# Kernel tuning notes

Hardware: AMD Instinct MI355X
Metric: run time of the kernel (lower is better)

The kernel has to match this reference:

```python
import jax, jax.numpy as jnp
import numpy as np
import math

NUM_LEVEL = 16
LEVEL_DIM = 2
BASE_RES = 16
LOG2_T = 19
LEVEL_SCALE = 1.38191288
N_POINTS = 262144

_PRIMES = np.array([1, 2654435761, 805459861], dtype=np.uint32)  # tiny-cuda-nn hash primes
_CORNERS = np.array([[(c >> d) & 1 for d in range(3)] for c in range(8)], dtype=np.uint32)  # [8,3]


def _grid_meta():
    # mirrors GridEncoder.get_grid_info: per-level table offsets (aligned to 8)
    max_len = 2 ** LOG2_T
    offs = []
    off = 0
    for i in range(NUM_LEVEL):
        res = int(np.ceil(BASE_RES * LEVEL_SCALE ** i))
        p = min(max_len, res ** 3)
        p = int(np.ceil(p / 8) * 8)
        offs.append(off)
        off += p
    offs.append(off)
    return offs


def setup_inputs() -> dict:
    key = jax.random.key(0)
    k1, k2 = jax.random.split(key)
    offs = _grid_meta()
    # raw coords in [-1, 1); forward maps (x+1)/2 -> [0, 1)
    input_means = jax.random.uniform(k1, (N_POINTS, 3), dtype=jnp.float32) * 2.0 - 1.0
    # embeddings.data.uniform_(-0.01, 0.01)
    embeddings = jax.random.uniform(k2, (offs[-1], LEVEL_DIM), dtype=jnp.float32) * 0.02 - 0.01
    return {"input_means": input_means, "embeddings": embeddings}


def _encode(input_means, embeddings):
    x = (input_means + 1.0) / 2.0  # [N,3] in [0,1]
    offs = _grid_meta()
    lg_scale = math.log2(LEVEL_SCALE)
    corners = jnp.asarray(_CORNERS)  # [8,3]
    primes = jnp.asarray(_PRIMES)    # [3]
    outs = []
    for l in range(NUM_LEVEL):
        hsize = offs[l + 1] - offs[l]                    # table rows this level
        scale = 2.0 ** (l * lg_scale) * BASE_RES - 1.0   # align_corners=True
        res = int(math.ceil(scale)) + 1                  # grid resolution
        table = embeddings[offs[l]:offs[l + 1]]          # [hsize, C]
        pos = x * scale                                  # align_corners -> no +0.5
        pg = jnp.floor(pos)
        frac = pos - pg                                  # [N,3]
        pgu = pg.astype(jnp.uint32)
        cpos = pgu[:, None, :] + corners[None]           # [N,8,3] corner coords
        if res ** 3 > hsize:
            # hashed level: xor of coord*prime (uint32 wraparound)
            h = cpos * primes
            idx = h[..., 0] ^ h[..., 1] ^ h[..., 2]
        else:
            # dense (tiled) level
            r = jnp.uint32(res)
            idx = cpos[..., 0] + cpos[..., 1] * r + cpos[..., 2] * r * r
        idx = (idx % jnp.uint32(hsize)).astype(jnp.int32)
        feats = table[idx]                               # [N,8,C] gather
        w = jnp.where(corners[None] == 1, frac[:, None, :], 1.0 - frac[:, None, :]).prod(-1)  # [N,8]
        outs.append(jnp.einsum('nk,nkc->nc', w, feats))  # trilinear interp
    # matches ot_encod.permute(1,0,2).reshape(N, L*C): level-major feature concat
    return jnp.concatenate(outs, axis=-1)                # [N, L*C]


def reference(input_means, embeddings):
    return _encode(input_means, embeddings)
```

## Files before the change

kernel.cpp:

```cpp
#include <hip/hip_runtime.h>
#include <cmath>

#define NPTS 262144
#define NLVL 16
#define NDENSE 5
#define NHASH 11
#define HASH_MASK 0x7FFFFu

struct MetaD { float scale[NDENSE]; unsigned off[NDENSE]; unsigned res[NDENSE]; };
struct MetaH { float scale[NHASH]; unsigned off[NHASH]; };

__global__ __launch_bounds__(256) void enc_dense(
    const float* __restrict__ means, const float* __restrict__ emb,
    float2* __restrict__ dst, int lvl_major, MetaD meta)
{
    const int p = blockIdx.x * 256 + threadIdx.x;
    const int l = blockIdx.y;

    const float x = (means[3 * p + 0] + 1.0f) * 0.5f;
    const float y = (means[3 * p + 1] + 1.0f) * 0.5f;
    const float z = (means[3 * p + 2] + 1.0f) * 0.5f;

    const float s      = meta.scale[l];
    const unsigned off = meta.off[l];
    const unsigned r   = meta.res[l];

    const float px = x * s, py = y * s, pz = z * s;
    const float gx = floorf(px), gy = floorf(py), gz = floorf(pz);
    const float fx = px - gx, fy = py - gy, fz = pz - gz;
    const unsigned ix = (unsigned)gx, iy = (unsigned)gy, iz = (unsigned)gz;

    const unsigned base = ix + iy * r + iz * r * r + off;
    const unsigned dy = r, dz = r * r;

    const float2* __restrict__ emb2 = (const float2*)emb;
    float2 f[8];
    f[0] = emb2[base];           f[1] = emb2[base + 1];
    f[2] = emb2[base + dy];      f[3] = emb2[base + dy + 1];
    f[4] = emb2[base + dz];      f[5] = emb2[base + dz + 1];
    f[6] = emb2[base + dz + dy]; f[7] = emb2[base + dz + dy + 1];

    const float wx0 = 1.0f - fx, wy0 = 1.0f - fy, wz0 = 1.0f - fz;
    const float w00 = wz0 * wy0, w01 = wz0 * fy, w10 = fz * wy0, w11 = fz * fy;
    const float a0 = w00 * (wx0 * f[0].x + fx * f[1].x) + w01 * (wx0 * f[2].x + fx * f[3].x)
                   + w10 * (wx0 * f[4].x + fx * f[5].x) + w11 * (wx0 * f[6].x + fx * f[7].x);
    const float a1 = w00 * (wx0 * f[0].y + fx * f[1].y) + w01 * (wx0 * f[2].y + fx * f[3].y)
                   + w10 * (wx0 * f[4].y + fx * f[5].y) + w11 * (wx0 * f[6].y + fx * f[7].y);

    const size_t di = lvl_major ? ((size_t)l * NPTS + p) : ((size_t)p * NLVL + l);
    dst[di] = make_float2(a0, a1);
}

__device__ __forceinline__ float2 hash_level(
    const float* __restrict__ emb, unsigned off, float s,
    float x, float y, float z)
{
    const float px = x * s, py = y * s, pz = z * s;
    const float gx = floorf(px), gy = floorf(py), gz = floorf(pz);
    const float fx = px - gx, fy = py - gy, fz = pz - gz;
    const unsigned ix = (unsigned)gx, iy = (unsigned)gy, iz = (unsigned)gz;

    const unsigned hy0 = iy * 2654435761u, hy1 = hy0 + 2654435761u;
    const unsigned hz0 = iz * 805459861u,  hz1 = hz0 + 805459861u;
    const unsigned hyz[4] = {hy0 ^ hz0, hy1 ^ hz0, hy0 ^ hz1, hy1 ^ hz1};

    const float wy0 = 1.0f - fy, wz0 = 1.0f - fz;
    const float wc[4] = {wy0 * wz0, fy * wz0, wy0 * fz, fy * fz};
    const float wx0 = 1.0f - fx;

    const float2* __restrict__ emb2 = (const float2*)emb;
    const float4* __restrict__ emb4 = (const float4*)emb;

    float a0 = 0.0f, a1 = 0.0f;
    if ((ix & 1u) == 0u) {
#pragma unroll
        for (int c = 0; c < 4; ++c) {
            const unsigned i0 = (ix ^ hyz[c]) & HASH_MASK;
            const float4 f = emb4[(off + (i0 & ~1u)) >> 1];
            const bool sw = (i0 & 1u);
            const float c0x = sw ? f.z : f.x, c0y = sw ? f.w : f.y;
            const float c1x = sw ? f.x : f.z, c1y = sw ? f.y : f.w;
            a0 += wc[c] * (wx0 * c0x + fx * c1x);
            a1 += wc[c] * (wx0 * c0y + fx * c1y);
        }
    } else {
#pragma unroll
        for (int c = 0; c < 4; ++c) {
            const unsigned i0 = (ix        ^ hyz[c]) & HASH_MASK;
            const unsigned i1 = ((ix + 1u) ^ hyz[c]) & HASH_MASK;
            const float2 f0 = emb2[off + i0];
            const float2 f1 = emb2[off + i1];
            a0 += wc[c] * (wx0 * f0.x + fx * f1.x);
            a1 += wc[c] * (wx0 * f0.y + fx * f1.y);
        }
    }
    return make_float2(a0, a1);
}

__global__ __launch_bounds__(256) void enc_hash(
    const float* __restrict__ means, const float* __restrict__ emb,
    float2* __restrict__ dst, int lvl_major, MetaH meta)
{
    const unsigned b = blockIdx.x;
    const unsigned xcd = b & 7u, slot = b >> 3;
    unsigned il, chunk;
    if (slot < 512u) { il = xcd; chunk = slot; }
    else {
        if (xcd >= 6u) return;
        il = 8u + (xcd >> 1);
        chunk = ((slot - 512u) << 1) | (xcd & 1u);
    }
    const float s      = meta.scale[il];
    const unsigned off = meta.off[il];
    const unsigned lvl = il + NDENSE;

    const unsigned p0 = chunk * 512u + threadIdx.x;

#pragma unroll
    for (int pp = 0; pp < 2; ++pp) {
        const unsigned p = p0 + pp * 256u;
        const float x = (means[3 * p + 0] + 1.0f) * 0.5f;
        const float y = (means[3 * p + 1] + 1.0f) * 0.5f;
        const float z = (means[3 * p + 2] + 1.0f) * 0.5f;
        const float2 a = hash_level(emb, off, s, x, y, z);
        const size_t di = lvl_major ? ((size_t)lvl * NPTS + p) : ((size_t)p * NLVL + lvl);
        dst[di] = a;
    }
}

__global__ __launch_bounds__(256) void transpose_out(
    const float2* __restrict__ ws, float* __restrict__ out)
{
    const int p = blockIdx.x * 256 + threadIdx.x;
    float4 o[8];
    float2* o2 = (float2*)o;
#pragma unroll
    for (int l = 0; l < NLVL; ++l)
        o2[l] = ws[(size_t)l * NPTS + p];
    float4* out4 = (float4*)(out + (size_t)p * (2 * NLVL));
#pragma unroll
    for (int k = 0; k < 8; ++k)
        out4[k] = o[k];
}

extern "C" void kernel_launch(void* const* d_in, const int* in_sizes, int n_in,
                              void* d_out, int out_size, void* d_ws, size_t ws_size,
                              hipStream_t stream)
{
    const float* means = (const float*)d_in[0];
    const float* emb   = (const float*)d_in[1];
    float* out         = (float*)d_out;

    MetaD md;
    MetaH mh;
    const double lg = log2(1.38191288);
    unsigned off = 0;
    for (int l = 0; l < NLVL; ++l) {
        const double scale_d = pow(2.0, (double)l * lg) * 16.0 - 1.0;
        const unsigned res_enc = (unsigned)ceil(scale_d) + 1u;

        const double gres_d = ceil(16.0 * pow(1.38191288, (double)l));
        unsigned long long r3 = (unsigned long long)gres_d;
        r3 = r3 * r3 * r3;
        unsigned long long pl = r3 < (1ull << 19) ? r3 : (1ull << 19);
        pl = (pl + 7ull) / 8ull * 8ull;

        if (l < NDENSE) {
            md.scale[l] = (float)scale_d;
            md.off[l]   = off;
            md.res[l]   = res_enc;
        } else {
            mh.scale[l - NDENSE] = (float)scale_d;
            mh.off[l - NDENSE]   = off;
        }
        off += (unsigned)pl;
    }

    const size_t ws_needed = (size_t)NLVL * NPTS * sizeof(float2);
    const bool use_ws = ws_size >= ws_needed;
    float2* dst = use_ws ? (float2*)d_ws : (float2*)out;
    const int lvl_major = use_ws ? 1 : 0;

    enc_dense<<<dim3(NPTS / 256, NDENSE, 1), 256, 0, stream>>>(means, emb, dst, lvl_major, md);
    enc_hash <<<dim3(8 * 768, 1, 1),          256, 0, stream>>>(means, emb, dst, lvl_major, mh);
    if (use_ws)
        transpose_out<<<NPTS / 256, 256, 0, stream>>>((const float2*)d_ws, out);
}
```

Before: 205.3 us.

## Batch two points per thread, use nontemporal loads/stores, rebalance hash block mapping

```diff
diff --git a/kernel.cpp b/kernel.cpp
--- a/kernel.cpp
+++ b/kernel.cpp
@@ -6,141 +6,140 @@
 #define NDENSE 5
 #define NHASH 11
 #define HASH_MASK 0x7FFFFu
+#define P2 2654435761u
+#define P3 805459861u
+
+typedef float v2f __attribute__((ext_vector_type(2)));
+typedef float v4f __attribute__((ext_vector_type(4)));
 
 struct MetaD { float scale[NDENSE]; unsigned off[NDENSE]; unsigned res[NDENSE]; };
 struct MetaH { float scale[NHASH]; unsigned off[NHASH]; };
 
+struct Pt { float x, y, z; };
+struct Prep { unsigned idx[8]; float fx, fy, fz; };
+
+__device__ __forceinline__ Pt load_pt(const float* __restrict__ means, int p) {
+    Pt q;
+    q.x = (__builtin_nontemporal_load(means + 3 * p + 0) + 1.0f) * 0.5f;
+    q.y = (__builtin_nontemporal_load(means + 3 * p + 1) + 1.0f) * 0.5f;
+    q.z = (__builtin_nontemporal_load(means + 3 * p + 2) + 1.0f) * 0.5f;
+    return q;
+}
+
+__device__ __forceinline__ Prep dprep(Pt q, float s, unsigned r, unsigned off) {
+    const float px = q.x * s, py = q.y * s, pz = q.z * s;
+    const float gx = floorf(px), gy = floorf(py), gz = floorf(pz);
+    Prep d;
+    d.fx = px - gx; d.fy = py - gy; d.fz = pz - gz;
+    const unsigned dy = r, dz = r * r;
+    const unsigned base = (unsigned)gx + (unsigned)gy * dy + (unsigned)gz * dz + off;
+    d.idx[0] = base;           d.idx[1] = base + 1;
+    d.idx[2] = base + dy;      d.idx[3] = base + dy + 1;
+    d.idx[4] = base + dz;      d.idx[5] = base + dz + 1;
+    d.idx[6] = base + dz + dy; d.idx[7] = base + dz + dy + 1;
+    return d;
+}
+
+__device__ __forceinline__ Prep hprep(Pt q, float s, unsigned off) {
+    const float px = q.x * s, py = q.y * s, pz = q.z * s;
+    const float gx = floorf(px), gy = floorf(py), gz = floorf(pz);
+    Prep d;
+    d.fx = px - gx; d.fy = py - gy; d.fz = pz - gz;
+    const unsigned ix = (unsigned)gx, iy = (unsigned)gy, iz = (unsigned)gz;
+    const unsigned hy0 = iy * P2, hy1 = hy0 + P2;
+    const unsigned hz0 = iz * P3, hz1 = hz0 + P3;
+    const unsigned h0 = hy0 ^ hz0, h1 = hy1 ^ hz0, h2 = hy0 ^ hz1, h3 = hy1 ^ hz1;
+    d.idx[0] = ((ix ^ h0) & HASH_MASK) + off; d.idx[1] = (((ix + 1u) ^ h0) & HASH_MASK) + off;
+    d.idx[2] = ((ix ^ h1) & HASH_MASK) + off; d.idx[3] = (((ix + 1u) ^ h1) & HASH_MASK) + off;
+    d.idx[4] = ((ix ^ h2) & HASH_MASK) + off; d.idx[5] = (((ix + 1u) ^ h2) & HASH_MASK) + off;
+    d.idx[6] = ((ix ^ h3) & HASH_MASK) + off; d.idx[7] = (((ix + 1u) ^ h3) & HASH_MASK) + off;
+    return d;
+}
+
+__device__ __forceinline__ v2f trilerp(const v2f* f, float fx, float fy, float fz) {
+    const float wx0 = 1.0f - fx, wy0 = 1.0f - fy, wz0 = 1.0f - fz;
+    const float w00 = wz0 * wy0, w01 = wz0 * fy, w10 = fz * wy0, w11 = fz * fy;
+    return w00 * (wx0 * f[0] + fx * f[1]) + w01 * (wx0 * f[2] + fx * f[3])
+         + w10 * (wx0 * f[4] + fx * f[5]) + w11 * (wx0 * f[6] + fx * f[7]);
+}
+
 __global__ __launch_bounds__(256) void enc_dense(
     const float* __restrict__ means, const float* __restrict__ emb,
-    float2* __restrict__ dst, int lvl_major, MetaD meta)
+    v2f* __restrict__ dst, int lvl_major, MetaD meta)
 {
-    const int p = blockIdx.x * 256 + threadIdx.x;
     const int l = blockIdx.y;
+    const int p0 = blockIdx.x * 512 + threadIdx.x;
+    const float s = meta.scale[l];
+    const unsigned off = meta.off[l];
+    const unsigned r = meta.res[l];
+    const v2f* __restrict__ emb2 = (const v2f*)emb;
 
-    const float x = (means[3 * p + 0] + 1.0f) * 0.5f;
-    const float y = (means[3 * p + 1] + 1.0f) * 0.5f;
-    const float z = (means[3 * p + 2] + 1.0f) * 0.5f;
+    const Prep A = dprep(load_pt(means, p0), s, r, off);
+    v2f fa[8];
+#pragma unroll
+    for (int k = 0; k < 8; ++k) fa[k] = emb2[A.idx[k]];
+    const Prep B = dprep(load_pt(means, p0 + 256), s, r, off);
+    v2f fb[8];
+#pragma unroll
+    for (int k = 0; k < 8; ++k) fb[k] = emb2[B.idx[k]];
 
-    const float s      = meta.scale[l];
-    const unsigned off = meta.off[l];
-    const unsigned r   = meta.res[l];
-
-    const float px = x * s, py = y * s, pz = z * s;
-    const float gx = floorf(px), gy = floorf(py), gz = floorf(pz);
-    const float fx = px - gx, fy = py - gy, fz = pz - gz;
-    const unsigned ix = (unsigned)gx, iy = (unsigned)gy, iz = (unsigned)gz;
-
-    const unsigned base = ix + iy * r + iz * r * r + off;
-    const unsigned dy = r, dz = r * r;
-
-    const float2* __restrict__ emb2 = (const float2*)emb;
-    float2 f[8];
-    f[0] = emb2[base];           f[1] = emb2[base + 1];
-    f[2] = emb2[base + dy];      f[3] = emb2[base + dy + 1];
-    f[4] = emb2[base + dz];      f[5] = emb2[base + dz + 1];
-    f[6] = emb2[base + dz + dy]; f[7] = emb2[base + dz + dy + 1];
-
-    const float wx0 = 1.0f - fx, wy0 = 1.0f - fy, wz0 = 1.0f - fz;
-    const float w00 = wz0 * wy0, w01 = wz0 * fy, w10 = fz * wy0, w11 = fz * fy;
-    const float a0 = w00 * (wx0 * f[0].x + fx * f[1].x) + w01 * (wx0 * f[2].x + fx * f[3].x)
-                   + w10 * (wx0 * f[4].x + fx * f[5].x) + w11 * (wx0 * f[6].x + fx * f[7].x);
-    const float a1 = w00 * (wx0 * f[0].y + fx * f[1].y) + w01 * (wx0 * f[2].y + fx * f[3].y)
-                   + w10 * (wx0 * f[4].y + fx * f[5].y) + w11 * (wx0 * f[6].y + fx * f[7].y);
-
-    const size_t di = lvl_major ? ((size_t)l * NPTS + p) : ((size_t)p * NLVL + l);
-    dst[di] = make_float2(a0, a1);
-}
-
-__device__ __forceinline__ float2 hash_level(
-    const float* __restrict__ emb, unsigned off, float s,
-    float x, float y, float z)
-{
-    const float px = x * s, py = y * s, pz = z * s;
-    const float gx = floorf(px), gy = floorf(py), gz = floorf(pz);
-    const float fx = px - gx, fy = py - gy, fz = pz - gz;
-    const unsigned ix = (unsigned)gx, iy = (unsigned)gy, iz = (unsigned)gz;
-
-    const unsigned hy0 = iy * 2654435761u, hy1 = hy0 + 2654435761u;
-    const unsigned hz0 = iz * 805459861u,  hz1 = hz0 + 805459861u;
-    const unsigned hyz[4] = {hy0 ^ hz0, hy1 ^ hz0, hy0 ^ hz1, hy1 ^ hz1};
-
-    const float wy0 = 1.0f - fy, wz0 = 1.0f - fz;
-    const float wc[4] = {wy0 * wz0, fy * wz0, wy0 * fz, fy * fz};
-    const float wx0 = 1.0f - fx;
-
-    const float2* __restrict__ emb2 = (const float2*)emb;
-    const float4* __restrict__ emb4 = (const float4*)emb;
-
-    float a0 = 0.0f, a1 = 0.0f;
-    if ((ix & 1u) == 0u) {
-#pragma unroll
-        for (int c = 0; c < 4; ++c) {
-            const unsigned i0 = (ix ^ hyz[c]) & HASH_MASK;
-            const float4 f = emb4[(off + (i0 & ~1u)) >> 1];
-            const bool sw = (i0 & 1u);
-            const float c0x = sw ? f.z : f.x, c0y = sw ? f.w : f.y;
-            const float c1x = sw ? f.x : f.z, c1y = sw ? f.y : f.w;
-            a0 += wc[c] * (wx0 * c0x + fx * c1x);
-            a1 += wc[c] * (wx0 * c0y + fx * c1y);
-        }
-    } else {
-#pragma unroll
-        for (int c = 0; c < 4; ++c) {
-            const unsigned i0 = (ix        ^ hyz[c]) & HASH_MASK;
-            const unsigned i1 = ((ix + 1u) ^ hyz[c]) & HASH_MASK;
-            const float2 f0 = emb2[off + i0];
-            const float2 f1 = emb2[off + i1];
-            a0 += wc[c] * (wx0 * f0.x + fx * f1.x);
-            a1 += wc[c] * (wx0 * f0.y + fx * f1.y);
-        }
-    }
-    return make_float2(a0, a1);
+    const v2f ra = trilerp(fa, A.fx, A.fy, A.fz);
+    const size_t diA = lvl_major ? ((size_t)l * NPTS + p0) : ((size_t)p0 * NLVL + l);
+    __builtin_nontemporal_store(ra, &dst[diA]);
+    const v2f rb = trilerp(fb, B.fx, B.fy, B.fz);
+    const size_t diB = lvl_major ? ((size_t)l * NPTS + p0 + 256) : ((size_t)(p0 + 256) * NLVL + l);
+    __builtin_nontemporal_store(rb, &dst[diB]);
 }
 
 __global__ __launch_bounds__(256) void enc_hash(
     const float* __restrict__ means, const float* __restrict__ emb,
-    float2* __restrict__ dst, int lvl_major, MetaH meta)
+    v2f* __restrict__ dst, int lvl_major, MetaH meta)
 {
     const unsigned b = blockIdx.x;
     const unsigned xcd = b & 7u, slot = b >> 3;
     unsigned il, chunk;
     if (slot < 512u) { il = xcd; chunk = slot; }
     else {
-        if (xcd >= 6u) return;
-        il = 8u + (xcd >> 1);
-        chunk = ((slot - 512u) << 1) | (xcd & 1u);
+        const unsigned g = xcd * 192u + (slot - 512u);
+        il = 8u + (g >> 9);
+        chunk = g & 511u;
     }
-    const float s      = meta.scale[il];
+    const float s = meta.scale[il];
     const unsigned off = meta.off[il];
     const unsigned lvl = il + NDENSE;
+    const int p0 = (int)(chunk * 512u + threadIdx.x);
+    const v2f* __restrict__ emb2 = (const v2f*)emb;
 
-    const unsigned p0 = chunk * 512u + threadIdx.x;
+    const Prep A = hprep(load_pt(means, p0), s, off);
+    v2f fa[8];
+#pragma unroll
+    for (int k = 0; k < 8; ++k) fa[k] = emb2[A.idx[k]];
+    const Prep B = hprep(load_pt(means, p0 + 256), s, off);
+    v2f fb[8];
+#pragma unroll
+    for (int k = 0; k < 8; ++k) fb[k] = emb2[B.idx[k]];
 
-#pragma unroll
-    for (int pp = 0; pp < 2; ++pp) {
-        const unsigned p = p0 + pp * 256u;
-        const float x = (means[3 * p + 0] + 1.0f) * 0.5f;
-        const float y = (means[3 * p + 1] + 1.0f) * 0.5f;
-        const float z = (means[3 * p + 2] + 1.0f) * 0.5f;
-        const float2 a = hash_level(emb, off, s, x, y, z);
-        const size_t di = lvl_major ? ((size_t)lvl * NPTS + p) : ((size_t)p * NLVL + lvl);
-        dst[di] = a;
-    }
+    const v2f ra = trilerp(fa, A.fx, A.fy, A.fz);
+    const size_t diA = lvl_major ? ((size_t)lvl * NPTS + p0) : ((size_t)p0 * NLVL + lvl);
+    __builtin_nontemporal_store(ra, &dst[diA]);
+    const v2f rb = trilerp(fb, B.fx, B.fy, B.fz);
+    const size_t diB = lvl_major ? ((size_t)lvl * NPTS + (p0 + 256)) : ((size_t)(p0 + 256) * NLVL + lvl);
+    __builtin_nontemporal_store(rb, &dst[diB]);
 }
 
 __global__ __launch_bounds__(256) void transpose_out(
-    const float2* __restrict__ ws, float* __restrict__ out)
+    const v2f* __restrict__ ws, float* __restrict__ out)
 {
     const int p = blockIdx.x * 256 + threadIdx.x;
-    float4 o[8];
-    float2* o2 = (float2*)o;
+    v4f o[8];
+    v2f* o2 = (v2f*)o;
 #pragma unroll
     for (int l = 0; l < NLVL; ++l)
-        o2[l] = ws[(size_t)l * NPTS + p];
-    float4* out4 = (float4*)(out + (size_t)p * (2 * NLVL));
+        o2[l] = __builtin_nontemporal_load(&ws[(size_t)l * NPTS + p]);
+    v4f* out4 = (v4f*)(out + (size_t)p * (2 * NLVL));
 #pragma unroll
     for (int k = 0; k < 8; ++k)
-        out4[k] = o[k];
+        __builtin_nontemporal_store(o[k], &out4[k]);
 }
 
 extern "C" void kernel_launch(void* const* d_in, const int* in_sizes, int n_in,
@@ -176,13 +175,13 @@
         off += (unsigned)pl;
     }
 
-    const size_t ws_needed = (size_t)NLVL * NPTS * sizeof(float2);
+    const size_t ws_needed = (size_t)NLVL * NPTS * sizeof(float) * 2;
     const bool use_ws = ws_size >= ws_needed;
-    float2* dst = use_ws ? (float2*)d_ws : (float2*)out;
+    v2f* dst = use_ws ? (v2f*)d_ws : (v2f*)out;
     const int lvl_major = use_ws ? 1 : 0;
 
-    enc_dense<<<dim3(NPTS / 256, NDENSE, 1), 256, 0, stream>>>(means, emb, dst, lvl_major, md);
-    enc_hash <<<dim3(8 * 768, 1, 1),          256, 0, stream>>>(means, emb, dst, lvl_major, mh);
+    enc_dense<<<dim3(NPTS / 512, NDENSE, 1), 256, 0, stream>>>(means, emb, dst, lvl_major, md);
+    enc_hash <<<dim3(8 * 704, 1, 1),          256, 0, stream>>>(means, emb, dst, lvl_major, mh);
     if (use_ws)
-        transpose_out<<<NPTS / 256, 256, 0, stream>>>((const float2*)d_ws, out);
+        transpose_out<<<NPTS / 256, 256, 0, stream>>>((const v2f*)d_ws, out);
 }
```

After: 247.2 us. 1.2x slower.
